# Kernel tuning notes

Hardware: AMD Instinct MI355X
Metric: run time of the kernel (lower is better)

Reference implementation:

```python
import jax, jax.numpy as jnp
import numpy as np

HIDDEN = 1024
NUM_HEADS = 16
HEAD_DIM = HIDDEN // NUM_HEADS  # 64
B, S = 4, 1024


def setup_inputs() -> dict:
    key = jax.random.key(0)
    ks = jax.random.split(key, 8)
    xavier = jax.nn.initializers.xavier_uniform()
    inputs = jax.random.normal(ks[0], (B, S, HIDDEN), dtype=jnp.float32)
    context = jax.random.normal(ks[1], (B, S, HIDDEN), dtype=jnp.float32)
    # multiplicative mask: 1 = attend, 0 = ignore (causal), broadcast over batch/heads
    mask = jnp.tril(jnp.ones((S, S), dtype=jnp.float32))[None, None, :, :]
    Wq = xavier(ks[2], (HIDDEN, HIDDEN), jnp.float32)
    bq = jnp.zeros((HIDDEN,), jnp.float32)
    Wk = xavier(ks[3], (HIDDEN, HEAD_DIM), jnp.float32)
    bk = jnp.zeros((HEAD_DIM,), jnp.float32)
    Wv = xavier(ks[4], (HIDDEN, HEAD_DIM), jnp.float32)
    bv = jnp.zeros((HEAD_DIM,), jnp.float32)
    Wo = xavier(ks[5], (HIDDEN, HIDDEN), jnp.float32)
    bo = jnp.zeros((HIDDEN,), jnp.float32)
    return {"inputs": inputs, "context": context, "mask": mask,
            "Wq": Wq, "bq": bq, "Wk": Wk, "bk": bk,
            "Wv": Wv, "bv": bv, "Wo": Wo, "bo": bo}


def reference(inputs, context, mask, Wq, bq, Wk, bk, Wv, bv, Wo, bo):
    query = inputs @ Wq + bq                      # (B, S, D)
    key = context @ Wk + bk                       # (B, S, D/H)
    value = context @ Wv + bv                     # (B, S, D/H)
    # MQA: broadcast single KV head to all query heads via interleaved repeat
    key = jnp.repeat(key, NUM_HEADS, axis=-1)     # (B, S, D)
    value = jnp.repeat(value, NUM_HEADS, axis=-1) # (B, S, D)
    bsz = query.shape[0]
    Lq, Lk = query.shape[1], key.shape[1]
    # faithful to original: plain reshape (not transpose) into heads
    qh = jnp.reshape(query, (bsz, NUM_HEADS, Lq, HEAD_DIM))
    kh = jnp.reshape(key, (bsz, NUM_HEADS, Lk, HEAD_DIM))
    vh = jnp.reshape(value, (bsz, NUM_HEADS, Lk, HEAD_DIM))
    # note: original scales by sqrt(key.shape[-1]) == sqrt(hidden_dim)
    scores = jnp.einsum('bhqd,bhkd->bhqk', qh, kh) / jnp.sqrt(jnp.float32(HIDDEN))
    scores = scores * mask                        # multiplicative mask
    attn = jax.nn.softmax(scores, axis=-1)        # (B, H, Lq, Lk)
    ctx = jnp.einsum('bhqk,bhkd->bhqd', attn, vh)
    ctx = jnp.reshape(ctx, (bsz, Lq, HIDDEN))
    outputs = ctx @ Wo + bo                       # (B, S, D)
    return outputs, attn
```

## Files before the change

### kernel.cpp

```cpp
#include <hip/hip_runtime.h>
#include <hip/hip_bf16.h>
#include <cstdint>

#define NHEADS 16
#define SEQ    1024
#define BATCH  4

typedef float vfloat4 __attribute__((ext_vector_type(4)));

__device__ __forceinline__ float wave_sum(float v){
  #pragma unroll
  for (int off = 32; off > 0; off >>= 1) v += __shfl_xor(v, off);
  return v;
}
__device__ __forceinline__ void nt_store4(float* p, float x, float y, float z, float w){
  vfloat4 v; v.x = x; v.y = y; v.z = z; v.w = w;
  __builtin_nontemporal_store(v, (vfloat4*)p);
}

__global__ __launch_bounds__(256) void prep_kernel(
    const float* __restrict__ Wq, const float* __restrict__ bq,
    const float* __restrict__ Wo,
    float* __restrict__ WqSum, float* __restrict__ bqSum, float* __restrict__ WoSum)
{
  const int blk = blockIdx.x, tid = threadIdx.x;
  if (blk < 256){
    const int c = blk * 4 + (tid >> 6), g = tid & 63;
    const float* p = &Wq[(size_t)c * 1024 + (g << 4)];
    float s = 0.f;
    #pragma unroll
    for (int f = 0; f < 16; ++f) s += p[f];
    WqSum[c * 64 + g] = s;
  } else if (blk < 320){
    const int g = blk - 256;
    for (int m = tid; m < 1024; m += 256){
      float s = 0.f;
      #pragma unroll
      for (int f = 0; f < 16; ++f) s += Wo[(size_t)((g << 4) + f) * 1024 + m];
      WoSum[g * 1024 + m] = s;
    }
  } else {
    if (tid < 64){
      float s = 0.f;
      #pragma unroll
      for (int f = 0; f < 16; ++f) s += bq[(tid << 4) + f];
      bqSum[tid] = s;
    }
  }
}

__global__ __launch_bounds__(256) void qkv_split(
    const float* __restrict__ inputs, const float* __restrict__ context,
    const float* __restrict__ WqSum,
    const float* __restrict__ Wk, const float* __restrict__ Wv,
    float* __restrict__ part)
{
  __shared__ float As[2][16][68];
  __shared__ float Bs[2][16][68];
  const int z = blockIdx.y, sz = blockIdx.z;
  const float* A = (z == 0) ? inputs : context;
  const float* B = (z == 0) ? WqSum : ((z == 1) ? Wk : Wv);
  const int m0 = blockIdx.x * 64;
  const int ks = sz << 8;
  const int tid = threadIdx.x;
  const int tx = tid & 15, ty = tid >> 4;
  const int arow = tid >> 2, acg = (tid & 3) << 2;
  const int brow = tid >> 4, bcg = (tid & 15) << 2;

  float4 av  = *(const float4*)&A[(size_t)(m0 + arow) * 1024 + ks + acg];
  float4 bvv = *(const float4*)&B[(size_t)(ks + brow) * 64 + bcg];
  As[0][acg + 0][arow] = av.x; As[0][acg + 1][arow] = av.y;
  As[0][acg + 2][arow] = av.z; As[0][acg + 3][arow] = av.w;
  *(float4*)&Bs[0][brow][bcg] = bvv;
  __syncthreads();

  float acc[4][4] = {};
  for (int t = 0; t < 16; ++t){
    const int cur = t & 1;
    if (t < 15){
      const int k0 = ks + ((t + 1) << 4);
      av  = *(const float4*)&A[(size_t)(m0 + arow) * 1024 + k0 + acg];
      bvv = *(const float4*)&B[(size_t)(k0 + brow) * 64 + bcg];
    }
    #pragma unroll
    for (int kk = 0; kk < 16; ++kk){
      const float4 a  = *(const float4*)&As[cur][kk][ty << 2];
      const float4 bb = *(const float4*)&Bs[cur][kk][tx << 2];
      const float a_[4] = {a.x, a.y, a.z, a.w};
      const float b_[4] = {bb.x, bb.y, bb.z, bb.w};
      #pragma unroll
      for (int i = 0; i < 4; ++i)
        #pragma unroll
        for (int j = 0; j < 4; ++j) acc[i][j] += a_[i] * b_[j];
    }
    if (t < 15){
      As[cur ^ 1][acg + 0][arow] = av.x; As[cur ^ 1][acg + 1][arow] = av.y;
      As[cur ^ 1][acg + 2][arow] = av.z; As[cur ^ 1][acg + 3][arow] = av.w;
      *(float4*)&Bs[cur ^ 1][brow][bcg] = bvv;
    }
    __syncthreads();
  }
  float* P = part + ((size_t)(z * 4 + sz) * 4096 + m0) * 64;
  #pragma unroll
  for (int i = 0; i < 4; ++i)
    *(float4*)&P[(size_t)((ty << 2) + i) * 64 + (tx << 2)] =
      make_float4(acc[i][0], acc[i][1], acc[i][2], acc[i][3]);
}

__global__ __launch_bounds__(256) void attn_fused(
    const float* __restrict__ part,
    const float* __restrict__ bqSum, const float* __restrict__ bk,
    const float* __restrict__ bv,
    const float* __restrict__ WoSum, const float* __restrict__ bo,
    float* __restrict__ outp, float* __restrict__ attnp)
{
  __shared__ float BmT[4][1032];
  __shared__ float VmT[4][1032];
  __shared__ float Aq[64][4];
  __shared__ float bsum16[16];
  __shared__ float SufT[4][5];
  __shared__ float CtxS[4][64];

  const int tid = threadIdx.x;
  const int qb = blockIdx.x;
  const int h  = blockIdx.y;
  const int b  = blockIdx.z;
  const int base = b * SEQ + h * 64;

  for (int idx = tid; idx < 4096; idx += 256){
    const int r = idx >> 6, c = idx & 63;
    const size_t off = (size_t)(base + r) * 64 + c;
    float kacc = bk[c], vacc = bv[c];
    #pragma unroll
    for (int s = 0; s < 4; ++s){
      kacc += part[(size_t)(4 + s) * 262144 + off];
      vacc += part[(size_t)(8 + s) * 262144 + off];
    }
    const int k = (r << 4) + (c >> 2), e = c & 3;
    BmT[e][k] = kacc;
    VmT[e][k] = vacc;
  }
  {
    const int p_l = tid >> 6, g = tid & 63;
    float qacc = bqSum[g];
    const size_t off = (size_t)(base + (qb << 2) + p_l) * 64 + g;
    #pragma unroll
    for (int s = 0; s < 4; ++s) qacc += part[(size_t)s * 262144 + off];
    Aq[(p_l << 4) + (g >> 2)][g & 3] = qacc;
  }
  __syncthreads();
  {
    const int pair = tid >> 4, sub = tid & 15;
    const int e = pair >> 2, jj = pair & 3;
    float s = 0.f;
    #pragma unroll
    for (int n = 0; n < 16; ++n) s += VmT[e][(jj << 8) + (n << 4) + sub];
    #pragma unroll
    for (int off2 = 8; off2 > 0; off2 >>= 1) s += __shfl_xor(s, off2);
    if (sub == 0) bsum16[pair] = s;
  }
  __syncthreads();
  if (tid < 4){
    float s = 0.f;
    SufT[tid][4] = 0.f;
    for (int jj = 3; jj >= 0; --jj){ s += bsum16[tid * 4 + jj]; SufT[tid][jj] = s; }
  }
  __syncthreads();

  const int wave = tid >> 6, lane = tid & 63;
  const int jdot  = (qb >> 2) + 1;
  const int ktail = jdot << 8;
  const float ztail = (float)(1024 - ktail);
  const float suf0 = SufT[0][jdot], suf1 = SufT[1][jdot];
  const float suf2 = SufT[2][jdot], suf3 = SufT[3][jdot];

  for (int i = 0; i < 16; i += 2){
    const int qlA = (wave << 4) + i;
    const int qA  = (qb << 6) + qlA, qB = qA + 1;
    const float4 aA = *(const float4*)&Aq[qlA][0];
    const float4 aB = *(const float4*)&Aq[qlA + 1][0];
    float4 svA[4], svB[4];
    float ZA = 0.f, ZB = 0.f;
    float cA0=0.f,cA1=0.f,cA2=0.f,cA3=0.f, cB0=0.f,cB1=0.f,cB2=0.f,cB3=0.f;
    #pragma unroll
    for (int j = 0; j < 4; ++j){
      if (j < jdot){
        const int k0 = (lane << 2) + (j << 8);
        const float4 b0 = *(const float4*)&BmT[0][k0];
        const float4 b1 = *(const float4*)&BmT[1][k0];
        const float4 b2 = *(const float4*)&BmT[2][k0];
        const float4 b3 = *(const float4*)&BmT[3][k0];
        float4 tA, tB;
        tA.x = (aA.x*b0.x + aA.y*b1.x + aA.z*b2.x + aA.w*b3.x) * 0.03125f;
        tA.y = (aA.x*b0.y + aA.y*b1.y + aA.z*b2.y + aA.w*b3.y) * 0.03125f;
        tA.z = (aA.x*b0.z + aA.y*b1.z + aA.z*b2.z + aA.w*b3.z) * 0.03125f;
        tA.w = (aA.x*b0.w + aA.y*b1.w + aA.z*b2.w + aA.w*b3.w) * 0.03125f;
        tB.x = (aB.x*b0.x + aB.y*b1.x + aB.z*b2.x + aB.w*b3.x) * 0.03125f;
        tB.y = (aB.x*b0.y + aB.y*b1.y + aB.z*b2.y + aB.w*b3.y) * 0.03125f;
        tB.z = (aB.x*b0.z + aB.y*b1.z + aB.z*b2.z + aB.w*b3.z) * 0.03125f;
        tB.w = (aB.x*b0.w + aB.y*b1.w + aB.z*b2.w + aB.w*b3.w) * 0.03125f;
        tA.x = (k0     <= qA) ? tA.x : 0.0f;
        tA.y = (k0 + 1 <= qA) ? tA.y : 0.0f;
        tA.z = (k0 + 2 <= qA) ? tA.z : 0.0f;
        tA.w = (k0 + 3 <= qA) ? tA.w : 0.0f;
        tB.x = (k0     <= qB) ? tB.x : 0.0f;
        tB.y = (k0 + 1 <= qB) ? tB.y : 0.0f;
        tB.z = (k0 + 2 <= qB) ? tB.z : 0.0f;
        tB.w = (k0 + 3 <= qB) ? tB.w : 0.0f;
        const float eA0 = __expf(tA.x), eA1 = __expf(tA.y);
        const float eA2 = __expf(tA.z), eA3 = __expf(tA.w);
        const float eB0 = __expf(tB.x), eB1 = __expf(tB.y);
        const float eB2 = __expf(tB.z), eB3 = __expf(tB.w);
        ZA += (eA0 + eA1) + (eA2 + eA3);
        ZB += (eB0 + eB1) + (eB2 + eB3);
        const float4 v0 = *(const float4*)&VmT[0][k0];
        const float4 v1 = *(const float4*)&VmT[1][k0];
        const float4 v2 = *(const float4*)&VmT[2][k0];
        const float4 v3 = *(const float4*)&VmT[3][k0];
        cA0 += eA0*v0.x + eA1*v0.y + eA2*v0.z + eA3*v0.w;
        cA1 += eA0*v1.x + eA1*v1.y + eA2*v1.z + eA3*v1.w;
        cA2 += eA0*v2.x + eA1*v2.y + eA2*v2.z + eA3*v2.w;
        cA3 += eA0*v3.x + eA1*v3.y + eA2*v3.z + eA3*v3.w;
        cB0 += eB0*v0.x + eB1*v0.y + eB2*v0.z + eB3*v0.w;
        cB1 += eB0*v1.x + eB1*v1.y + eB2*v1.z + eB3*v1.w;
        cB2 += eB0*v2.x + eB1*v2.y + eB2*v2.z + eB3*v2.w;
        cB3 += eB0*v3.x + eB1*v3.y + eB2*v3.z + eB3*v3.w;
        svA[j] = make_float4(eA0, eA1, eA2, eA3);
        svB[j] = make_float4(eB0, eB1, eB2, eB3);
      }
    }
    const float ZAt = wave_sum(ZA) + ztail;
    const float ZBt = wave_sum(ZB) + ztail;
    cA0 = wave_sum(cA0) + suf0; cA1 = wave_sum(cA1) + suf1;
    cA2 = wave_sum(cA2) + suf2; cA3 = wave_sum(cA3) + suf3;
    cB0 = wave_sum(cB0) + suf0; cB1 = wave_sum(cB1) + suf1;
    cB2 = wave_sum(cB2) + suf2; cB3 = wave_sum(cB3) + suf3;
    const float invZA = 1.0f / ZAt, invZB = 1.0f / ZBt;

    float* rowA = attnp + (((size_t)(b * NHEADS + h) << 10) + (size_t)qA) * 1024;
    float* rowB = rowA + 1024;
    #pragma unroll
    for (int j = 0; j < 4; ++j){
      if (j < jdot){
        const int k0 = (lane << 2) + (j << 8);
        nt_store4(rowA + k0, svA[j].x * invZA, svA[j].y * invZA,
                             svA[j].z * invZA, svA[j].w * invZA);
        nt_store4(rowB + k0, svB[j].x * invZB, svB[j].y * invZB,
                             svB[j].z * invZB, svB[j].w * invZB);
      }
    }
    for (int rr = 0; rr < 4 - jdot; ++rr){
      const int kf = ktail + (rr << 8) + (lane << 2);
      nt_store4(rowA + kf, invZA, invZA, invZA, invZA);
      nt_store4(rowB + kf, invZB, invZB, invZB, invZB);
    }
    if (lane == 0){
      *(float4*)&CtxS[wave][i << 2] =
        make_float4(cA0 * invZA, cA1 * invZA, cA2 * invZA, cA3 * invZA);
      *(float4*)&CtxS[wave][(i + 1) << 2] =
        make_float4(cB0 * invZB, cB1 * invZB, cB2 * invZB, cB3 * invZB);
    }
  }
  __syncthreads();

  {
    const int i = tid >> 6, t = tid & 63;
    float4 acc[4];
    #pragma unroll
    for (int jj = 0; jj < 4; ++jj) acc[jj] = make_float4(0.f, 0.f, 0.f, 0.f);
    for (int g = 0; g < 64; ++g){
      const float cg = CtxS[i][g];
      const float* wrow = &WoSum[(size_t)g * 1024 + (t << 2)];
      #pragma unroll
      for (int jj = 0; jj < 4; ++jj){
        const float4 w = *(const float4*)&wrow[jj << 8];
        acc[jj].x += cg * w.x; acc[jj].y += cg * w.y;
        acc[jj].z += cg * w.z; acc[jj].w += cg * w.w;
      }
    }
    const size_t R = (size_t)(base + (qb << 2) + i);
    #pragma unroll
    for (int jj = 0; jj < 4; ++jj){
      const float4 bov = *(const float4*)&bo[(jj << 8) + (t << 2)];
      nt_store4(&outp[R * 1024 + (jj << 8) + (t << 2)],
                acc[jj].x + bov.x, acc[jj].y + bov.y,
                acc[jj].z + bov.z, acc[jj].w + bov.w);
    }
  }
}

extern "C" void kernel_launch(void* const* d_in, const int* in_sizes, int n_in,
                              void* d_out, int out_size, void* d_ws, size_t ws_size,
                              hipStream_t stream)
{
  const float* inputs  = (const float*)d_in[0];
  const float* context = (const float*)d_in[1];
  const float* Wq = (const float*)d_in[3];
  const float* bq = (const float*)d_in[4];
  const float* Wk = (const float*)d_in[5];
  const float* bk = (const float*)d_in[6];
  const float* Wv = (const float*)d_in[7];
  const float* bv = (const float*)d_in[8];
  const float* Wo = (const float*)d_in[9];
  const float* bo = (const float*)d_in[10];

  float* outp  = (float*)d_out;
  float* attnp = outp + (size_t)BATCH * SEQ * 1024;

  float* ws    = (float*)d_ws;
  float* WqSum = ws;
  float* bqSum = ws + 65536;
  float* WoSum = ws + 65600;
  float* part  = ws + 131136;

  prep_kernel<<<dim3(321), dim3(256), 0, stream>>>(Wq, bq, Wo, WqSum, bqSum, WoSum);
  qkv_split <<<dim3(64, 3, 4), dim3(256), 0, stream>>>(inputs, context, WqSum,
                                                       Wk, Wv, part);
  attn_fused<<<dim3(16, 16, 4), dim3(256), 0, stream>>>(part, bqSum, bk, bv,
                                                        WoSum, bo, outp, attnp);
}
```

Baseline: 124.1 us.

## Split output projection out of attention kernel into a tiled GEMM

```diff
diff --git a/kernel.cpp b/kernel.cpp
--- a/kernel.cpp
+++ b/kernel.cpp
@@ -107,22 +107,20 @@
       make_float4(acc[i][0], acc[i][1], acc[i][2], acc[i][3]);
 }
 
-__global__ __launch_bounds__(256) void attn_fused(
+__global__ __launch_bounds__(256) void attn_kernel(
     const float* __restrict__ part,
     const float* __restrict__ bqSum, const float* __restrict__ bk,
     const float* __restrict__ bv,
-    const float* __restrict__ WoSum, const float* __restrict__ bo,
-    float* __restrict__ outp, float* __restrict__ attnp)
+    float* __restrict__ Ctx, float* __restrict__ attnp)
 {
   __shared__ float BmT[4][1032];
   __shared__ float VmT[4][1032];
   __shared__ float Aq[64][4];
   __shared__ float bsum16[16];
   __shared__ float SufT[4][5];
-  __shared__ float CtxS[4][64];
 
   const int tid = threadIdx.x;
-  const int qb = blockIdx.x;
+  const int qb = (blockIdx.x + (blockIdx.z << 2)) & 15;
   const int h  = blockIdx.y;
   const int b  = blockIdx.z;
   const int base = b * SEQ + h * 64;
@@ -255,37 +253,54 @@
       nt_store4(rowB + kf, invZB, invZB, invZB, invZB);
     }
     if (lane == 0){
-      *(float4*)&CtxS[wave][i << 2] =
+      *(float4*)&Ctx[(size_t)(base + (qA >> 4)) * 64 + ((qA & 15) << 2)] =
         make_float4(cA0 * invZA, cA1 * invZA, cA2 * invZA, cA3 * invZA);
-      *(float4*)&CtxS[wave][(i + 1) << 2] =
+      *(float4*)&Ctx[(size_t)(base + (qB >> 4)) * 64 + ((qB & 15) << 2)] =
         make_float4(cB0 * invZB, cB1 * invZB, cB2 * invZB, cB3 * invZB);
     }
   }
-  __syncthreads();
-
-  {
-    const int i = tid >> 6, t = tid & 63;
-    float4 acc[4];
-    #pragma unroll
-    for (int jj = 0; jj < 4; ++jj) acc[jj] = make_float4(0.f, 0.f, 0.f, 0.f);
-    for (int g = 0; g < 64; ++g){
-      const float cg = CtxS[i][g];
-      const float* wrow = &WoSum[(size_t)g * 1024 + (t << 2)];
+}
+
+__global__ __launch_bounds__(256) void out_gemm(
+    const float* __restrict__ Ctx, const float* __restrict__ WoSum,
+    const float* __restrict__ bo, float* __restrict__ outp)
+{
+  __shared__ float Cs[64][68];
+  __shared__ float Ws[64][128];
+  const int tid = threadIdx.x;
+  const int m0 = blockIdx.x * 64, n0 = blockIdx.y * 128;
+
+  for (int t = tid; t < 1024; t += 256){
+    const int row = t >> 4, c4 = (t & 15) << 2;
+    const float4 v = *(const float4*)&Ctx[(size_t)(m0 + row) * 64 + c4];
+    Cs[c4 + 0][row] = v.x; Cs[c4 + 1][row] = v.y;
+    Cs[c4 + 2][row] = v.z; Cs[c4 + 3][row] = v.w;
+  }
+  for (int t = tid; t < 2048; t += 256){
+    const int row = t >> 5, c4 = (t & 31) << 2;
+    *(float4*)&Ws[row][c4] = *(const float4*)&WoSum[(size_t)row * 1024 + n0 + c4];
+  }
+  __syncthreads();
+
+  const int tx = tid & 31, ty = tid >> 5;
+  float acc[8][4] = {};
+  for (int kk = 0; kk < 64; ++kk){
+    const float4 bb = *(const float4*)&Ws[kk][tx << 2];
+    const float4 a0 = *(const float4*)&Cs[kk][ty << 3];
+    const float4 a1 = *(const float4*)&Cs[kk][(ty << 3) + 4];
+    const float a_[8] = {a0.x, a0.y, a0.z, a0.w, a1.x, a1.y, a1.z, a1.w};
+    const float b_[4] = {bb.x, bb.y, bb.z, bb.w};
+    #pragma unroll
+    for (int i = 0; i < 8; ++i)
       #pragma unroll
-      for (int jj = 0; jj < 4; ++jj){
-        const float4 w = *(const float4*)&wrow[jj << 8];
-        acc[jj].x += cg * w.x; acc[jj].y += cg * w.y;
-        acc[jj].z += cg * w.z; acc[jj].w += cg * w.w;
-      }
-    }
-    const size_t R = (size_t)(base + (qb << 2) + i);
-    #pragma unroll
-    for (int jj = 0; jj < 4; ++jj){
-      const float4 bov = *(const float4*)&bo[(jj << 8) + (t << 2)];
-      nt_store4(&outp[R * 1024 + (jj << 8) + (t << 2)],
-                acc[jj].x + bov.x, acc[jj].y + bov.y,
-                acc[jj].z + bov.z, acc[jj].w + bov.w);
-    }
+      for (int j = 0; j < 4; ++j) acc[i][j] += a_[i] * b_[j];
+  }
+  const float4 bov = *(const float4*)&bo[n0 + (tx << 2)];
+  #pragma unroll
+  for (int i = 0; i < 8; ++i){
+    nt_store4(&outp[(size_t)(m0 + (ty << 3) + i) * 1024 + n0 + (tx << 2)],
+              acc[i][0] + bov.x, acc[i][1] + bov.y,
+              acc[i][2] + bov.z, acc[i][3] + bov.w);
   }
 }
 
@@ -311,11 +326,13 @@
   float* WqSum = ws;
   float* bqSum = ws + 65536;
   float* WoSum = ws + 65600;
-  float* part  = ws + 131136;
+  float* Ctx   = ws + 131136;
+  float* part  = ws + 393280;
 
   prep_kernel<<<dim3(321), dim3(256), 0, stream>>>(Wq, bq, Wo, WqSum, bqSum, WoSum);
   qkv_split <<<dim3(64, 3, 4), dim3(256), 0, stream>>>(inputs, context, WqSum,
                                                        Wk, Wv, part);
-  attn_fused<<<dim3(16, 16, 4), dim3(256), 0, stream>>>(part, bqSum, bk, bv,
-                                                        WoSum, bo, outp, attnp);
-}
+  attn_kernel<<<dim3(16, 16, 4), dim3(256), 0, stream>>>(part, bqSum, bk, bv,
+                                                         Ctx, attnp);
+  out_gemm  <<<dim3(64, 8), dim3(256), 0, stream>>>(Ctx, WoSum, bo, outp);
+}
```

After: 117.2 us. 1.06x faster.
